# Performance work log

Hardware: AMD Instinct MI355X
Metric: run time of the kernel (lower is better)

Reference implementation:

```python
import jax, jax.numpy as jnp
import numpy as np

THETAS = np.linspace(0.5, 1.5, 9)


def _interp_nearest(x, theta):
    # torch F.interpolate(mode='nearest') on last dim: src = floor(dst * in/out)
    in_len = x.shape[-1]
    out_len = int(np.floor(in_len * theta))
    idx = np.floor(np.arange(out_len) * (in_len / out_len)).astype(np.int32)
    return x[..., idx]


def _argaug(x, y):
    # x, y: (B, T, idim)
    B, T, idim_q = y.shape
    pad = idim_q - 1
    sim_max_global = jnp.zeros((B, T), x.dtype)
    x_aug = None
    for theta in THETAS:
        x_s = _interp_nearest(x, float(theta))          # (B, T, idim_k)
        idim_k = x_s.shape[-1]
        key_pad = jnp.pad(x_s, ((0, 0), (0, 0), (pad, pad)))
        n_shift = idim_k + idim_q - 1
        win_idx = np.arange(n_shift)[:, None] + np.arange(idim_q)[None, :]  # (S, q)
        trunk = key_pad[:, :, win_idx]                  # (B, T, S, q)
        denom = jnp.linalg.norm(y, axis=-1)[..., None] * jnp.linalg.norm(trunk, axis=-1)
        sim = jnp.einsum('btq,btsq->bts', y, trunk) / denom  # (B, T, S)
        sim_max = jnp.max(sim, axis=-1)
        sim_idx = jnp.argmax(sim, axis=-1)              # (B, T) int
        x_shift = jnp.take_along_axis(trunk, sim_idx[..., None, None], axis=2)[:, :, 0, :]
        mask = sim_max_global < sim_max
        sim_max_global = jnp.where(mask, sim_max, sim_max_global)
        if x_aug is None:
            x_aug = x_shift
        else:
            x_aug = jnp.where(mask[..., None], x_shift, x_aug)
    return x_aug, sim_max_global


def setup_inputs() -> dict:
    key = jax.random.key(0)
    ks = jax.random.split(key, 4)
    B, T, idim, hdim, odim = 4, 256, 256, 1024, 256
    x = jax.random.normal(ks[0], (B, T, idim), jnp.float32)
    y = jax.random.normal(ks[1], (B, T, odim), jnp.float32)
    W1 = jax.random.normal(ks[2], (idim, hdim), jnp.float32) * (1.0 / np.sqrt(idim))
    b1 = jnp.zeros((hdim,), jnp.float32)
    W2 = jax.random.normal(ks[3], (hdim, odim), jnp.float32) * (1.0 / np.sqrt(hdim))
    b2 = jnp.zeros((odim,), jnp.float32)
    # hg kernel: gaussian over hidden index, normalized to max 1 -> P(mask==1)
    w = np.exp(-0.5 * (np.arange(hdim, dtype=np.float32) / 430.0) ** 2)
    freq = jnp.asarray(w / w.max(), jnp.float32)
    return {"x": x, "y": y, "W1": W1, "b1": b1, "W2": W2, "b2": b2, "freq": freq}


def reference(x, y, W1, b1, W2, b2, freq):
    ignore_out = 0.0
    x_aug, _ = _argaug(x, y)                 # (B, T, idim)
    idim = x.shape[-1]
    odim = y.shape[-1]
    xf = x_aug.reshape(-1, idim)             # (N, idim)
    yf = y.reshape(-1, odim)                 # (N, odim)
    hdim = W1.shape[1]
    # freq_mask: multinomial over (1-w, w) per hidden unit == bernoulli(w)
    mk = jax.random.bernoulli(jax.random.key(42), freq, (xf.shape[0], hdim))
    h = (xf @ W1 + b1) * mk.astype(xf.dtype)
    out = h @ W2 + b2 + xf                   # (N, odim)
    # NetLoss: masked elementwise MSE, mean over non-ignored entries
    m = yf == ignore_out
    denom = (~m).astype(xf.dtype).sum()
    loss = jnp.where(m, 0.0, (out - yf) ** 2).sum() / denom
    return loss, out
```

## Files before the change

### kernel.cpp

```cpp
#include <hip/hip_runtime.h>
#include <stdint.h>

#define ROWS 1024
#define IDIM 256
#define HDIM 1024

__device__ __forceinline__ uint32_t rotl32(uint32_t x, int r){ return (x<<r)|(x>>(32-r)); }

__device__ __forceinline__ void threefry(uint32_t x0, uint32_t x1, uint32_t& o0, uint32_t& o1){
  const uint32_t k0 = 0u, k1 = 42u;
  const uint32_t k2 = 0x1BD11BDAu ^ k0 ^ k1;
  x0 += k0; x1 += k1;
#define TFR(r) { x0 += x1; x1 = rotl32(x1, r); x1 ^= x0; }
  TFR(13) TFR(15) TFR(26) TFR(6)  x0 += k1; x1 += k2 + 1u;
  TFR(17) TFR(29) TFR(16) TFR(24) x0 += k2; x1 += k0 + 2u;
  TFR(13) TFR(15) TFR(26) TFR(6)  x0 += k0; x1 += k1 + 3u;
  TFR(17) TFR(29) TFR(16) TFR(24) x0 += k1; x1 += k2 + 4u;
  TFR(13) TFR(15) TFR(26) TFR(6)  x0 += k2; x1 += k0 + 5u;
#undef TFR
  o0 = x0; o1 = x1;
}

__global__ __launch_bounds__(256) void mask_kernel(const float* __restrict__ freq,
                                                   float* __restrict__ mkf)
{
  uint32_t i = blockIdx.x * 256u + threadIdx.x;
  uint32_t o0, o1;
  threefry(0u, i, o0, o1);
  uint32_t bits = o0 ^ o1;
  float u = __uint_as_float((bits >> 9) | 0x3F800000u) - 1.0f;
  mkf[i] = (u < freq[i & 1023u]) ? 1.0f : 0.0f;
}

__global__ __launch_bounds__(256) void argaug_kernel(const float* __restrict__ x,
                                                     const float* __restrict__ y,
                                                     float* __restrict__ xaug)
{
  __shared__ float  xs[IDIM];
  __shared__ float  ys[IDIM];
  __shared__ float  kp[1024];
  __shared__ double rv[256];
  __shared__ int    rk[256];
  __shared__ double cand_v[128];
  __shared__ int    cand_k[128];
  __shared__ int    list[128];
  __shared__ int    cnt;

  const int tid  = threadIdx.x;
  const int wave = tid >> 6;
  const int lane = tid & 63;
  const int row  = blockIdx.x;

  xs[tid] = x[row * IDIM + tid];
  ys[tid] = y[row * IDIM + tid];
  if (tid == 0) cnt = 0;
  const int sbase = 192 * wave + 3 * lane;

  float s0[9], s1[9], s2[9];

#pragma unroll
  for (int t = 0; t < 9; ++t) {
    const int OL = 128 + 32 * t;
    const double ratio = 256.0 / (double)OL;

    __syncthreads();
#pragma unroll
    for (int ii = 0; ii < 4; ++ii) {
      int i = tid + 256 * ii;
      float v = 0.0f;
      int j = i - 255;
      if (j >= 0 && j < OL) v = xs[(int)floor((double)j * ratio)];
      kp[i] = v;
    }
    __syncthreads();

    float a0=0.f,a1=0.f,a2=0.f, n0=0.f,n1=0.f,n2=0.f;
    const int qlo = (wave == 0) ? 64 : 0;
    const int qhi = min(256, 255 + OL - 192 * wave);
    if (qhi > qlo) {
      int p = sbase + qlo;
      float c0 = kp[p], c1 = kp[p+1], c2 = kp[p+2], c3;
      for (int q = qlo; q < qhi; q += 4) {
        float4 y4 = *(const float4*)&ys[q];
        a0 += y4.x*c0; n0 += c0*c0;
        a1 += y4.x*c1; n1 += c1*c1;
        a2 += y4.x*c2; n2 += c2*c2;
        c3 = kp[p+3];
        a0 += y4.y*c1; a1 += y4.y*c2; a2 += y4.y*c3; n0 += c1*c1; n1 += c2*c2; n2 += c3*c3;
        c0 = kp[p+4];
        a0 += y4.z*c2; a1 += y4.z*c3; a2 += y4.z*c0; n0 += c2*c2; n1 += c3*c3; n2 += c0*c0;
        c1 = kp[p+5];
        a0 += y4.w*c3; a1 += y4.w*c0; a2 += y4.w*c1; n0 += c3*c3; n1 += c0*c0; n2 += c1*c1;
        c2 = kp[p+6];
        p += 4;
      }
    }
    const int nsh = OL + 255;
    s0[t] = (sbase     < nsh && n0 > 0.f) ? a0 * __frsqrt_rn(n0) : -1.0e30f;
    s1[t] = (sbase + 1 < nsh && n1 > 0.f) ? a1 * __frsqrt_rn(n1) : -1.0e30f;
    s2[t] = (sbase + 2 < nsh && n2 > 0.f) ? a2 * __frsqrt_rn(n2) : -1.0e30f;
  }
  __syncthreads();

  {
    float gm = -1.0e30f;
#pragma unroll
    for (int t = 0; t < 9; ++t) gm = fmaxf(gm, fmaxf(s0[t], fmaxf(s1[t], s2[t])));
    rv[tid] = (double)gm;
  }
  __syncthreads();
  for (int off = 128; off > 0; off >>= 1) {
    if (tid < off) rv[tid] = fmax(rv[tid], rv[tid+off]);
    __syncthreads();
  }
  const float gmax32 = (float)rv[0];
  __syncthreads();
  rv[tid] = (double)fmaxf(s0[0], fmaxf(s1[0], s2[0]));
  __syncthreads();
  for (int off = 128; off > 0; off >>= 1) {
    if (tid < off) rv[tid] = fmax(rv[tid], rv[tid+off]);
    __syncthreads();
  }
  const float t0max32 = (float)rv[0];

  const float gthr = gmax32  - 1.0e-3f;
  const float tthr = t0max32 - 1.0e-3f;
#pragma unroll
  for (int t = 0; t < 9; ++t) {
#pragma unroll
    for (int r = 0; r < 3; ++r) {
      float v = (r == 0) ? s0[t] : (r == 1) ? s1[t] : s2[t];
      if (v >= gthr || (t == 0 && v >= tthr)) {
        int id = atomicAdd(&cnt, 1);
        if (id < 128) list[id] = (t << 10) | (sbase + r);
      }
    }
  }
  __syncthreads();
  const int m = min(cnt, 128);

  for (int c = wave; c < m; c += 4) {
    const int slot = list[c];
    const int tt = slot >> 10, ss = slot & 1023;
    const int OLr = 128 + 32 * tt;
    const double ratior = 256.0 / (double)OLr;
    double a64 = 0.0, n64 = 0.0;
#pragma unroll
    for (int k = 0; k < 4; ++k) {
      int q = 4 * lane + k;
      int j = ss + q - 255;
      if (j >= 0 && j < OLr) {
        double cc = (double)xs[(int)floor((double)j * ratior)];
        a64 += (double)ys[q] * cc;
        n64 += cc * cc;
      }
    }
#pragma unroll
    for (int d = 1; d < 64; d <<= 1) {
      a64 += __shfl_xor(a64, d, 64);
      n64 += __shfl_xor(n64, d, 64);
    }
    if (lane == 0) {
      cand_v[c] = (n64 > 0.0) ? a64 / sqrt(n64) : -1.0e300;
      cand_k[c] = slot;
    }
  }
  __syncthreads();

  rv[tid] = (tid < m) ? cand_v[tid] : -1.0e300;
  rk[tid] = (tid < m) ? cand_k[tid] : 0x3FFFFFFF;
  __syncthreads();
  for (int off = 128; off > 0; off >>= 1) {
    if (tid < off) {
      double v2 = rv[tid+off]; int k2 = rk[tid+off];
      if (v2 > rv[tid] || (v2 == rv[tid] && k2 < rk[tid])) { rv[tid] = v2; rk[tid] = k2; }
    }
    __syncthreads();
  }
  const double gbest = rv[0];
  const int    gk    = rk[0];
  __syncthreads();

  rv[tid] = (tid < m && (cand_k[tid] >> 10) == 0) ? cand_v[tid] : -1.0e300;
  rk[tid] = (tid < m) ? cand_k[tid] : 0x3FFFFFFF;
  __syncthreads();
  for (int off = 128; off > 0; off >>= 1) {
    if (tid < off) {
      double v2 = rv[tid+off]; int k2 = rk[tid+off];
      if (v2 > rv[tid] || (v2 == rv[tid] && k2 < rk[tid])) { rv[tid] = v2; rk[tid] = k2; }
    }
    __syncthreads();
  }
  const int wk = (gbest > 0.0) ? gk : rk[0];

  const int tb = wk >> 10, sb = wk & 1023;
  const int OLb = 128 + 32 * tb;
  const double ratiob = 256.0 / (double)OLb;
  int j = sb + tid - 255;
  float v = 0.0f;
  if (j >= 0 && j < OLb) v = xs[(int)floor((double)j * ratiob)];
  xaug[row * IDIM + tid] = v;
}

__global__ __launch_bounds__(256) void gemm1_kernel(const float* __restrict__ A,
                                                    const float* __restrict__ W1,
                                                    const float* __restrict__ b1,
                                                    const float* __restrict__ mkf,
                                                    float* __restrict__ h)
{
  __shared__ float As[32][68];
  __shared__ float Bs[32][68];
  const int tid = threadIdx.x;
  const int m0 = blockIdx.x * 64;
  const int n0 = blockIdx.y * 64;
  const int tx = tid & 15, ty = tid >> 4;
  float acc[4][4] = {};

  for (int kt = 0; kt < 256; kt += 32) {
#pragma unroll
    for (int jj = 0; jj < 8; ++jj) {
      int f = tid + 256*jj;
      As[f & 31][f >> 5] = A[(m0 + (f >> 5)) * 256 + kt + (f & 31)];
    }
#pragma unroll
    for (int jj = 0; jj < 8; ++jj) {
      int f = tid + 256*jj;
      Bs[f >> 6][f & 63] = W1[(kt + (f >> 6)) * 1024 + n0 + (f & 63)];
    }
    __syncthreads();
#pragma unroll
    for (int kk = 0; kk < 32; ++kk) {
      float4 a4 = *(const float4*)&As[kk][4*ty];
      float4 b4 = *(const float4*)&Bs[kk][4*tx];
      acc[0][0] += a4.x*b4.x; acc[0][1] += a4.x*b4.y; acc[0][2] += a4.x*b4.z; acc[0][3] += a4.x*b4.w;
      acc[1][0] += a4.y*b4.x; acc[1][1] += a4.y*b4.y; acc[1][2] += a4.y*b4.z; acc[1][3] += a4.y*b4.w;
      acc[2][0] += a4.z*b4.x; acc[2][1] += a4.z*b4.y; acc[2][2] += a4.z*b4.z; acc[2][3] += a4.z*b4.w;
      acc[3][0] += a4.w*b4.x; acc[3][1] += a4.w*b4.y; acc[3][2] += a4.w*b4.z; acc[3][3] += a4.w*b4.w;
    }
    __syncthreads();
  }

  float4 bias = *(const float4*)&b1[n0 + 4*tx];
#pragma unroll
  for (int r = 0; r < 4; ++r) {
    int mm = m0 + 4*ty + r;
    float4 mk4 = *(const float4*)&mkf[mm * 1024 + n0 + 4*tx];
    float4 o;
    o.x = (acc[r][0] + bias.x) * mk4.x;
    o.y = (acc[r][1] + bias.y) * mk4.y;
    o.z = (acc[r][2] + bias.z) * mk4.z;
    o.w = (acc[r][3] + bias.w) * mk4.w;
    *(float4*)&h[mm * 1024 + n0 + 4*tx] = o;
  }
}

__global__ __launch_bounds__(256) void gemm2_kernel(const float* __restrict__ h,
                                                    const float* __restrict__ W2,
                                                    float* __restrict__ out_acc)
{
  __shared__ float As[32][68];
  __shared__ float Bs[32][68];
  const int tid = threadIdx.x;
  const int m0 = blockIdx.x * 64;
  const int n0 = blockIdx.y * 64;
  const int kz = blockIdx.z * 256;
  const int tx = tid & 15, ty = tid >> 4;
  float acc[4][4] = {};

  for (int kt = 0; kt < 256; kt += 32) {
#pragma unroll
    for (int jj = 0; jj < 8; ++jj) {
      int f = tid + 256*jj;
      As[f & 31][f >> 5] = h[(m0 + (f >> 5)) * 1024 + kz + kt + (f & 31)];
    }
#pragma unroll
    for (int jj = 0; jj < 8; ++jj) {
      int f = tid + 256*jj;
      Bs[f >> 6][f & 63] = W2[(kz + kt + (f >> 6)) * 256 + n0 + (f & 63)];
    }
    __syncthreads();
#pragma unroll
    for (int kk = 0; kk < 32; ++kk) {
      float4 a4 = *(const float4*)&As[kk][4*ty];
      float4 b4 = *(const float4*)&Bs[kk][4*tx];
      acc[0][0] += a4.x*b4.x; acc[0][1] += a4.x*b4.y; acc[0][2] += a4.x*b4.z; acc[0][3] += a4.x*b4.w;
      acc[1][0] += a4.y*b4.x; acc[1][1] += a4.y*b4.y; acc[1][2] += a4.y*b4.z; acc[1][3] += a4.y*b4.w;
      acc[2][0] += a4.z*b4.x; acc[2][1] += a4.z*b4.y; acc[2][2] += a4.z*b4.z; acc[2][3] += a4.z*b4.w;
      acc[3][0] += a4.w*b4.x; acc[3][1] += a4.w*b4.y; acc[3][2] += a4.w*b4.z; acc[3][3] += a4.w*b4.w;
    }
    __syncthreads();
  }

#pragma unroll
  for (int r = 0; r < 4; ++r)
#pragma unroll
    for (int c = 0; c < 4; ++c)
      unsafeAtomicAdd(&out_acc[(m0 + 4*ty + r) * 256 + n0 + 4*tx + c], acc[r][c]);
}

__global__ __launch_bounds__(256) void finalize_kernel(const float* __restrict__ out_acc,
                                                       const float* __restrict__ b2,
                                                       const float* __restrict__ xaug,
                                                       const float* __restrict__ yref,
                                                       float* __restrict__ d_out,
                                                       double* __restrict__ loss_acc,
                                                       unsigned int* __restrict__ cnt_acc)
{
  __shared__ double sred[4];
  __shared__ unsigned int cred[4];
  int i = blockIdx.x * 256 + threadIdx.x;
  int n = i & 255;
  float v = out_acc[i] + b2[n] + xaug[i];
  d_out[1 + i] = v;
  float yv = yref[i];
  bool valid = (yv != 0.0f);
  float df = v - yv;
  double lsd = valid ? (double)df * (double)df : 0.0;
#pragma unroll
  for (int off = 32; off > 0; off >>= 1) lsd += __shfl_down(lsd, off, 64);
  unsigned long long bal = __ballot(valid);
  int wvx = threadIdx.x >> 6, ln = threadIdx.x & 63;
  if (ln == 0) { sred[wvx] = lsd; cred[wvx] = (unsigned int)__popcll(bal); }
  __syncthreads();
  if (threadIdx.x == 0) {
    double s = sred[0] + sred[1] + sred[2] + sred[3];
    unsigned int c = cred[0] + cred[1] + cred[2] + cred[3];
    atomicAdd(loss_acc, s);
    atomicAdd(cnt_acc, c);
  }
}

__global__ void loss_kernel(const double* __restrict__ loss_acc,
                            const unsigned int* __restrict__ cnt_acc,
                            float* __restrict__ d_out)
{
  d_out[0] = (float)(loss_acc[0] / (double)cnt_acc[0]);
}

extern "C" void kernel_launch(void* const* d_in, const int* in_sizes, int n_in,
                              void* d_out, int out_size, void* d_ws, size_t ws_size,
                              hipStream_t stream) {
  const float* x    = (const float*)d_in[0];
  const float* y    = (const float*)d_in[1];
  const float* W1   = (const float*)d_in[2];
  const float* b1   = (const float*)d_in[3];
  const float* W2   = (const float*)d_in[4];
  const float* b2   = (const float*)d_in[5];
  const float* freq = (const float*)d_in[6];
  float* out = (float*)d_out;

  char* ws = (char*)d_ws;
  float*  xaug = (float*)(ws);
  float*  h    = (float*)(ws + (1u<<20));
  float*  mkf  = (float*)(ws + 5u*(1u<<20));
  float*  oacc = (float*)(ws + 9u*(1u<<20));
  double* lacc = (double*)(ws + 10u*(1u<<20));
  unsigned int* cacc = (unsigned int*)(ws + 10u*(1u<<20) + 8u);

  hipMemsetAsync(ws + 9u*(1u<<20), 0, (1u<<20) + 16u, stream);

  mask_kernel  <<<4096, 256, 0, stream>>>(freq, mkf);
  argaug_kernel<<<1024, 256, 0, stream>>>(x, y, xaug);
  gemm1_kernel <<<dim3(16,16),  256, 0, stream>>>(xaug, W1, b1, mkf, h);
  gemm2_kernel <<<dim3(16,4,4), 256, 0, stream>>>(h, W2, oacc);
  finalize_kernel<<<1024, 256, 0, stream>>>(oacc, b2, xaug, y, out, lacc, cacc);
  loss_kernel  <<<1, 1, 0, stream>>>(lacc, cacc, out);
}
```

Before: 250.5 us.

## Fuse mask generation into GEMM1 epilogue and restructure argaug shift staging

```diff
diff --git a/kernel.cpp b/kernel.cpp
--- a/kernel.cpp
+++ b/kernel.cpp
@@ -1,13 +1,11 @@
 #include <hip/hip_runtime.h>
 #include <stdint.h>
 
-#define ROWS 1024
 #define IDIM 256
-#define HDIM 1024
 
 __device__ __forceinline__ uint32_t rotl32(uint32_t x, int r){ return (x<<r)|(x>>(32-r)); }
 
-__device__ __forceinline__ void threefry(uint32_t x0, uint32_t x1, uint32_t& o0, uint32_t& o1){
+__device__ __forceinline__ uint32_t threefry_xor(uint32_t x0, uint32_t x1){
   const uint32_t k0 = 0u, k1 = 42u;
   const uint32_t k2 = 0x1BD11BDAu ^ k0 ^ k1;
   x0 += k0; x1 += k1;
@@ -18,18 +16,7 @@
   TFR(17) TFR(29) TFR(16) TFR(24) x0 += k1; x1 += k2 + 4u;
   TFR(13) TFR(15) TFR(26) TFR(6)  x0 += k2; x1 += k0 + 5u;
 #undef TFR
-  o0 = x0; o1 = x1;
-}
-
-__global__ __launch_bounds__(256) void mask_kernel(const float* __restrict__ freq,
-                                                   float* __restrict__ mkf)
-{
-  uint32_t i = blockIdx.x * 256u + threadIdx.x;
-  uint32_t o0, o1;
-  threefry(0u, i, o0, o1);
-  uint32_t bits = o0 ^ o1;
-  float u = __uint_as_float((bits >> 9) | 0x3F800000u) - 1.0f;
-  mkf[i] = (u < freq[i & 1023u]) ? 1.0f : 0.0f;
+  return x0 ^ x1;
 }
 
 __global__ __launch_bounds__(256) void argaug_kernel(const float* __restrict__ x,
@@ -38,7 +25,7 @@
 {
   __shared__ float  xs[IDIM];
   __shared__ float  ys[IDIM];
-  __shared__ float  kp[1024];
+  __shared__ float  ks[4672];
   __shared__ double rv[256];
   __shared__ int    rk[256];
   __shared__ double cand_v[128];
@@ -50,62 +37,67 @@
   const int wave = tid >> 6;
   const int lane = tid & 63;
   const int row  = blockIdx.x;
+  const int OFF[9] = {0, 391, 814, 1269, 1756, 2275, 2826, 3409, 4024};
 
   xs[tid] = x[row * IDIM + tid];
   ys[tid] = y[row * IDIM + tid];
   if (tid == 0) cnt = 0;
-  const int sbase = 192 * wave + 3 * lane;
-
-  float s0[9], s1[9], s2[9];
+  __syncthreads();
 
 #pragma unroll
   for (int t = 0; t < 9; ++t) {
     const int OL = 128 + 32 * t;
     const double ratio = 256.0 / (double)OL;
-
-    __syncthreads();
-#pragma unroll
-    for (int ii = 0; ii < 4; ++ii) {
-      int i = tid + 256 * ii;
+    const int base = OFF[t];
+    for (int p = tid; p < 263 + OL; p += 256) {
       float v = 0.0f;
-      int j = i - 255;
+      int j = p - 255;
       if (j >= 0 && j < OL) v = xs[(int)floor((double)j * ratio)];
-      kp[i] = v;
-    }
-    __syncthreads();
+      ks[base + p] = v;
+    }
+  }
+  __syncthreads();
+
+  float sA[9], sB[9], sC[9];
+
+#pragma unroll
+  for (int t = 0; t < 9; ++t) {
+    const int OL  = 128 + 32 * t;
+    const int nsh = OL + 255;
+    const int b   = (wave + t) & 3;
+    const int sb  = 192 * b + 3 * lane;
+    const int qlo = (b == 0) ? 64 : 0;
+    const int qhi = min(256, nsh - sb);
+    const int base = OFF[t] + sb;
 
     float a0=0.f,a1=0.f,a2=0.f, n0=0.f,n1=0.f,n2=0.f;
-    const int qlo = (wave == 0) ? 64 : 0;
-    const int qhi = min(256, 255 + OL - 192 * wave);
     if (qhi > qlo) {
-      int p = sbase + qlo;
-      float c0 = kp[p], c1 = kp[p+1], c2 = kp[p+2], c3;
+      int p = base + qlo;
+      float c0 = ks[p], c1 = ks[p+1], c2 = ks[p+2], c3;
       for (int q = qlo; q < qhi; q += 4) {
         float4 y4 = *(const float4*)&ys[q];
         a0 += y4.x*c0; n0 += c0*c0;
         a1 += y4.x*c1; n1 += c1*c1;
         a2 += y4.x*c2; n2 += c2*c2;
-        c3 = kp[p+3];
+        c3 = ks[p+3];
         a0 += y4.y*c1; a1 += y4.y*c2; a2 += y4.y*c3; n0 += c1*c1; n1 += c2*c2; n2 += c3*c3;
-        c0 = kp[p+4];
+        c0 = ks[p+4];
         a0 += y4.z*c2; a1 += y4.z*c3; a2 += y4.z*c0; n0 += c2*c2; n1 += c3*c3; n2 += c0*c0;
-        c1 = kp[p+5];
+        c1 = ks[p+5];
         a0 += y4.w*c3; a1 += y4.w*c0; a2 += y4.w*c1; n0 += c3*c3; n1 += c0*c0; n2 += c1*c1;
-        c2 = kp[p+6];
+        c2 = ks[p+6];
         p += 4;
       }
     }
-    const int nsh = OL + 255;
-    s0[t] = (sbase     < nsh && n0 > 0.f) ? a0 * __frsqrt_rn(n0) : -1.0e30f;
-    s1[t] = (sbase + 1 < nsh && n1 > 0.f) ? a1 * __frsqrt_rn(n1) : -1.0e30f;
-    s2[t] = (sbase + 2 < nsh && n2 > 0.f) ? a2 * __frsqrt_rn(n2) : -1.0e30f;
-  }
-  __syncthreads();
+    sA[t] = (sb     < nsh && n0 > 0.f) ? a0 * __frsqrt_rn(n0) : -1.0e30f;
+    sB[t] = (sb + 1 < nsh && n1 > 0.f) ? a1 * __frsqrt_rn(n1) : -1.0e30f;
+    sC[t] = (sb + 2 < nsh && n2 > 0.f) ? a2 * __frsqrt_rn(n2) : -1.0e30f;
+  }
 
   {
     float gm = -1.0e30f;
 #pragma unroll
-    for (int t = 0; t < 9; ++t) gm = fmaxf(gm, fmaxf(s0[t], fmaxf(s1[t], s2[t])));
+    for (int t = 0; t < 9; ++t) gm = fmaxf(gm, fmaxf(sA[t], fmaxf(sB[t], sC[t])));
     rv[tid] = (double)gm;
   }
   __syncthreads();
@@ -115,7 +107,7 @@
   }
   const float gmax32 = (float)rv[0];
   __syncthreads();
-  rv[tid] = (double)fmaxf(s0[0], fmaxf(s1[0], s2[0]));
+  rv[tid] = (double)fmaxf(sA[0], fmaxf(sB[0], sC[0]));
   __syncthreads();
   for (int off = 128; off > 0; off >>= 1) {
     if (tid < off) rv[tid] = fmax(rv[tid], rv[tid+off]);
@@ -127,12 +119,14 @@
   const float tthr = t0max32 - 1.0e-3f;
 #pragma unroll
   for (int t = 0; t < 9; ++t) {
+    const int b  = (wave + t) & 3;
+    const int sb = 192 * b + 3 * lane;
 #pragma unroll
     for (int r = 0; r < 3; ++r) {
-      float v = (r == 0) ? s0[t] : (r == 1) ? s1[t] : s2[t];
+      float v = (r == 0) ? sA[t] : (r == 1) ? sB[t] : sC[t];
       if (v >= gthr || (t == 0 && v >= tthr)) {
         int id = atomicAdd(&cnt, 1);
-        if (id < 128) list[id] = (t << 10) | (sbase + r);
+        if (id < 128) list[id] = (t << 10) | (sb + r);
       }
     }
   }
@@ -193,10 +187,10 @@
   }
   const int wk = (gbest > 0.0) ? gk : rk[0];
 
-  const int tb = wk >> 10, sb = wk & 1023;
+  const int tb = wk >> 10, sb2 = wk & 1023;
   const int OLb = 128 + 32 * tb;
   const double ratiob = 256.0 / (double)OLb;
-  int j = sb + tid - 255;
+  int j = sb2 + tid - 255;
   float v = 0.0f;
   if (j >= 0 && j < OLb) v = xs[(int)floor((double)j * ratiob)];
   xaug[row * IDIM + tid] = v;
@@ -205,9 +199,20 @@
 __global__ __launch_bounds__(256) void gemm1_kernel(const float* __restrict__ A,
                                                     const float* __restrict__ W1,
                                                     const float* __restrict__ b1,
-                                                    const float* __restrict__ mkf,
-                                                    float* __restrict__ h)
+                                                    const float* __restrict__ freq,
+                                                    float* __restrict__ h,
+                                                    float* __restrict__ oacc,
+                                                    double* __restrict__ lacc,
+                                                    unsigned int* __restrict__ cacc,
+                                                    unsigned int* __restrict__ done)
 {
+  {
+    const int gz = (blockIdx.y * 16 + blockIdx.x) * 256 + threadIdx.x;
+    float4 z; z.x = z.y = z.z = z.w = 0.f;
+    *(float4*)&oacc[gz * 4] = z;
+    if (gz == 0) { *lacc = 0.0; *cacc = 0u; *done = 0u; }
+  }
+
   __shared__ float As[32][68];
   __shared__ float Bs[32][68];
   const int tid = threadIdx.x;
@@ -241,15 +246,22 @@
   }
 
   float4 bias = *(const float4*)&b1[n0 + 4*tx];
+  float4 fq4  = *(const float4*)&freq[n0 + 4*tx];
 #pragma unroll
   for (int r = 0; r < 4; ++r) {
-    int mm = m0 + 4*ty + r;
-    float4 mk4 = *(const float4*)&mkf[mm * 1024 + n0 + 4*tx];
+    const int mm = m0 + 4*ty + r;
+    const uint32_t ib = (uint32_t)(mm * 1024 + n0 + 4*tx);
     float4 o;
-    o.x = (acc[r][0] + bias.x) * mk4.x;
-    o.y = (acc[r][1] + bias.y) * mk4.y;
-    o.z = (acc[r][2] + bias.z) * mk4.z;
-    o.w = (acc[r][3] + bias.w) * mk4.w;
+    {
+      float u = __uint_as_float((threefry_xor(0u, ib+0u) >> 9) | 0x3F800000u) - 1.0f;
+      o.x = (acc[r][0] + bias.x) * ((u < fq4.x) ? 1.0f : 0.0f);
+      u = __uint_as_float((threefry_xor(0u, ib+1u) >> 9) | 0x3F800000u) - 1.0f;
+      o.y = (acc[r][1] + bias.y) * ((u < fq4.y) ? 1.0f : 0.0f);
+      u = __uint_as_float((threefry_xor(0u, ib+2u) >> 9) | 0x3F800000u) - 1.0f;
+      o.z = (acc[r][2] + bias.z) * ((u < fq4.z) ? 1.0f : 0.0f);
+      u = __uint_as_float((threefry_xor(0u, ib+3u) >> 9) | 0x3F800000u) - 1.0f;
+      o.w = (acc[r][3] + bias.w) * ((u < fq4.w) ? 1.0f : 0.0f);
+    }
     *(float4*)&h[mm * 1024 + n0 + 4*tx] = o;
   }
 }
@@ -303,8 +315,9 @@
                                                        const float* __restrict__ xaug,
                                                        const float* __restrict__ yref,
                                                        float* __restrict__ d_out,
-                                                       double* __restrict__ loss_acc,
-                                                       unsigned int* __restrict__ cnt_acc)
+                                                       double* __restrict__ lacc,
+                                                       unsigned int* __restrict__ cacc,
+                                                       unsigned int* __restrict__ done)
 {
   __shared__ double sred[4];
   __shared__ unsigned int cred[4];
@@ -325,16 +338,16 @@
   if (threadIdx.x == 0) {
     double s = sred[0] + sred[1] + sred[2] + sred[3];
     unsigned int c = cred[0] + cred[1] + cred[2] + cred[3];
-    atomicAdd(loss_acc, s);
-    atomicAdd(cnt_acc, c);
-  }
-}
-
-__global__ void loss_kernel(const double* __restrict__ loss_acc,
-                            const unsigned int* __restrict__ cnt_acc,
-                            float* __restrict__ d_out)
-{
-  d_out[0] = (float)(loss_acc[0] / (double)cnt_acc[0]);
+    atomicAdd(lacc, s);
+    atomicAdd(cacc, c);
+    __threadfence();
+    unsigned int old = atomicAdd(done, 1u);
+    if (old == gridDim.x - 1u) {
+      double tot = atomicAdd(lacc, 0.0);
+      unsigned int cc = atomicAdd(cacc, 0u);
+      d_out[0] = (float)(tot / (double)cc);
+    }
+  }
 }
 
 extern "C" void kernel_launch(void* const* d_in, const int* in_sizes, int n_in,
@@ -352,17 +365,13 @@
   char* ws = (char*)d_ws;
   float*  xaug = (float*)(ws);
   float*  h    = (float*)(ws + (1u<<20));
-  float*  mkf  = (float*)(ws + 5u*(1u<<20));
   float*  oacc = (float*)(ws + 9u*(1u<<20));
   double* lacc = (double*)(ws + 10u*(1u<<20));
   unsigned int* cacc = (unsigned int*)(ws + 10u*(1u<<20) + 8u);
-
-  hipMemsetAsync(ws + 9u*(1u<<20), 0, (1u<<20) + 16u, stream);
-
-  mask_kernel  <<<4096, 256, 0, stream>>>(freq, mkf);
+  unsigned int* done = (unsigned int*)(ws + 10u*(1u<<20) + 12u);
+
   argaug_kernel<<<1024, 256, 0, stream>>>(x, y, xaug);
-  gemm1_kernel <<<dim3(16,16),  256, 0, stream>>>(xaug, W1, b1, mkf, h);
+  gemm1_kernel <<<dim3(16,16),  256, 0, stream>>>(xaug, W1, b1, freq, h, oacc, lacc, cacc, done);
   gemm2_kernel <<<dim3(16,4,4), 256, 0, stream>>>(h, W2, oacc);
-  finalize_kernel<<<1024, 256, 0, stream>>>(oacc, b2, xaug, y, out, lacc, cacc);
-  loss_kernel  <<<1, 1, 0, stream>>>(lacc, cacc, out);
-}
+  finalize_kernel<<<1024, 256, 0, stream>>>(oacc, b2, xaug, y, out, lacc, cacc, done);
+}
```

Measured after the change: 240.2 us. -4.1%, faster.
